# Kernel tuning notes

Measured on AMD Instinct MI355X. Metric: run time of the kernel, lower is better.

Reference implementation:

```python
import jax, jax.numpy as jnp
import numpy as np

WINDOWLEN = 8      # init arg windowlen
LOSS_THR = 120.0   # init arg losss
Q_BITS = 16


def ste_round(x):
    # Round with straight-through estimator (matches torch Round.apply)
    return x + jax.lax.stop_gradient(jnp.round(x) - x)


def delta_comp(x):
    # left-neighbor delta along width, zero-padded first column
    x_left = jnp.pad(x[:, :, :, :-1], ((0, 0), (0, 0), (0, 0), (1, 0)))
    return x - x_left, x_left


def part_quant(x, mx, mn, bw):
    neq = mx != mn
    denom = jnp.where(neq, mx - mn, jnp.ones((), x.dtype))
    scale = jnp.where(neq, (2.0 ** bw - 1.0) / denom, jnp.ones((), x.dtype))
    q = jnp.where(neq, ste_round((x - mn) * scale), x)
    return q, 1.0 / scale, jnp.where(neq, mn, jnp.zeros((), x.dtype))


def part_quant1(x, mx, bw):
    # en == 1 branch of the original
    lsb = 2.0 ** (ste_round(jnp.log2(mx / 2.0 ** (bw - 1))) + 1.0)
    return ste_round(x / lsb) * lsb


def setup_inputs() -> dict:
    key = jax.random.key(0)
    x = jax.random.normal(key, (1, 32, 1024, 1024), dtype=jnp.float32)
    return {"x": x}


def reference(x):
    w = WINDOWLEN
    batch, imgnum, height, width = x.shape
    # NOTE: the original also computes an 8-bit quantized delta (x_256) and
    # 2/4/8-bit masks, but these only feed print-statistics, never the output,
    # so they are omitted here.
    xd, x_left = delta_comp(x)
    In_max = xd.max()
    In_min = xd.min()
    q, s, m = part_quant(xd, In_max, In_min, Q_BITS)
    x1 = q * s + m  # dequantized delta
    Wb, Hb = width // w, height // w
    # --- block decomposition (replicates the torch reshape/permute chain) ---
    b = x1.reshape(batch, imgnum, height, Wb, w).transpose(0, 1, 3, 2, 4)
    c = b.reshape(batch, imgnum, Wb, Hb, w, w).transpose(0, 2, 3, 1, 4, 5)
    d = c.reshape(batch, Wb, Hb, imgnum, w * w).transpose(0, 1, 2, 4, 3)[0]  # [Wb,Hb,w*w,I]
    d1 = d.transpose(0, 1, 3, 2)  # [Wb,Hb,I,w*w]
    # --- 3x3 least-squares: fit each frame block from frames 0,1 + const ---
    a1 = d1[:, :, 0:1, :]
    a2 = d1[:, :, 1:2, :]
    a_base = jnp.concatenate([a1, a2, jnp.ones_like(a1)], axis=2)  # [Wb,Hb,3,w*w]
    degen = ((a1.max(3)[:, :, 0] - a1.min(3)[:, :, 0] < 1e-6)
             & (a2.max(3)[:, :, 0] - a2.min(3)[:, :, 0] < 1e-6))  # [Wb,Hb]
    a_t = a_base.transpose(0, 1, 3, 2)
    AT_A = a_base @ a_t  # [Wb,Hb,3,3]
    eye3 = jnp.eye(3, dtype=x.dtype)
    AT_A = jnp.where((jnp.linalg.det(AT_A) == 0)[..., None, None], eye3, AT_A)
    AT_A_inv = jnp.linalg.inv(AT_A)
    base = AT_A_inv @ a_base          # [Wb,Hb,3,w*w]
    p = base @ d                      # [Wb,Hb,3,I]
    r = a_t @ p                       # [Wb,Hb,w*w,I]
    r1 = part_quant1(r.transpose(0, 1, 3, 2), In_max, Q_BITS)  # [Wb,Hb,I,w*w]
    # --- per-(block,frame) accept/reject by MSE threshold ---
    loss_sum = ((d1 - r1) ** 2).sum(-1)  # [Wb,Hb,I]
    loss_sum = jnp.where(degen[..., None], LOSS_THR + 1.0, loss_sum)
    sel = loss_sum <= LOSS_THR
    rr = jnp.where(sel[..., None], r1, d1)
    rr = jnp.where(degen[..., None, None], d1, rr)  # rr[mask] = d1[mask]
    # --- reassemble image (reverse reshape chain) ---
    rr = rr.reshape(Wb, Hb, imgnum, w, w).transpose(2, 1, 3, 0, 4)
    rr = rr.reshape(imgnum, height, width)[None]
    return rr + x_left  # delta_dcom
```

## Files before the change

### kernel.cpp

```cpp
#include <hip/hip_runtime.h>
#include <math.h>

#define IMGN 32
#define HT 1024
#define WD 1024
#define IMG_STRIDE (HT*WD)
#define LOSS_THR_F 120.0f
#define MMX_BLOCKS 4096

#define IST 68
#define SST (32*IST + 8)

__global__ __launch_bounds__(256) void k_minmax(const float* __restrict__ x,
                                                float* __restrict__ wsf){
  const int lane = threadIdx.x & 63;
  const int wave_id = (blockIdx.x*256 + threadIdx.x) >> 6;
  const float4* x4 = (const float4*)x;
  const int base4 = wave_id * 512;

  float4 v[8];
  #pragma unroll
  for (int j = 0; j < 8; ++j) v[j] = x4[base4 + j*64 + lane];

  float lmin = INFINITY, lmax = -INFINITY;
  #pragma unroll
  for (int j = 0; j < 8; ++j){
    float lf = __shfl_up(v[j].w, 1);
    float carry = (j == 0 || j == 4) ? 0.0f : __shfl(v[j-1].w, 63);
    if (lane == 0) lf = carry;
    float d0 = v[j].x - lf,      d1 = v[j].y - v[j].x;
    float d2 = v[j].z - v[j].y,  d3 = v[j].w - v[j].z;
    lmin = fminf(lmin, fminf(fminf(d0, d1), fminf(d2, d3)));
    lmax = fmaxf(lmax, fmaxf(fmaxf(d0, d1), fmaxf(d2, d3)));
  }
  #pragma unroll
  for (int off = 32; off; off >>= 1){
    lmin = fminf(lmin, __shfl_xor(lmin, off));
    lmax = fmaxf(lmax, __shfl_xor(lmax, off));
  }
  __shared__ float smin[4], smax[4];
  int wv = threadIdx.x >> 6;
  if (lane == 0){ smin[wv] = lmin; smax[wv] = lmax; }
  __syncthreads();
  if (threadIdx.x == 0){
    wsf[2*blockIdx.x]   = fminf(fminf(smin[0], smin[1]), fminf(smin[2], smin[3]));
    wsf[2*blockIdx.x+1] = fmaxf(fmaxf(smax[0], smax[1]), fmaxf(smax[2], smax[3]));
  }
}

__global__ __launch_bounds__(256) void k_reduce(float* __restrict__ wsf){
  int t = threadIdx.x;
  float mn = INFINITY, mx = -INFINITY;
  #pragma unroll
  for (int j = 0; j < MMX_BLOCKS/256; ++j){
    float2 p = ((const float2*)wsf)[t + 256*j];
    mn = fminf(mn, p.x); mx = fmaxf(mx, p.y);
  }
  #pragma unroll
  for (int off = 32; off; off >>= 1){
    mn = fminf(mn, __shfl_xor(mn, off));
    mx = fmaxf(mx, __shfl_xor(mx, off));
  }
  __shared__ float smin[4], smax[4];
  int wv = t >> 6;
  if ((t & 63) == 0){ smin[wv] = mn; smax[wv] = mx; }
  __syncthreads();
  if (t == 0){
    wsf[2*MMX_BLOCKS]   = fminf(fminf(smin[0], smin[1]), fminf(smin[2], smin[3]));
    wsf[2*MMX_BLOCKS+1] = fmaxf(fmaxf(smax[0], smax[1]), fmaxf(smax[2], smax[3]));
  }
}

__global__ __launch_bounds__(512) void k_main(const float* __restrict__ x,
                                              float* __restrict__ out,
                                              const float* __restrict__ wsf){
  __shared__ __align__(16) float dsh[4*SST];
  __shared__ float s_inv[4][9];
  __shared__ int   s_degen[4];

  const int tid = threadIdx.x;
  const int bid = blockIdx.x;
  const int xcd = bid & 7;
  const int jj  = bid >> 3;
  const int hb  = xcd*16 + (jj >> 5);
  const int cb  = jj & 31;
  const int row0 = hb << 3;
  const int col0 = cb << 5;

  const float mn = wsf[2*MMX_BLOCKS];
  const float mx = wsf[2*MMX_BLOCKS+1];
  const bool  neq = (mx != mn);
  const float scale = neq ? (65535.0f / (mx - mn)) : 1.0f;
  const float sinv  = 1.0f / scale;
  const float moff  = neq ? mn : 0.0f;
  const float e1   = rintf(log2f(mx * (1.0f/32768.0f))) + 1.0f;
  const float lsb  = exp2f(e1);
  const float ilsb = exp2f(-e1);

  const int rem = tid & 63;
  const int r   = rem >> 3;
  const int fi  = rem & 7;
  const int i0  = tid >> 6;
  const int sB0 = fi >> 1;
  const int p1  = (r << 3) + ((fi & 1) << 2);
  const int lbase0 = sB0*SST + i0*IST + p1;
  const int gc0 = col0 + (fi << 2);
  const size_t elt0 = (size_t)i0*IMG_STRIDE + (size_t)(row0+r)*WD + gc0;

  float4 keep[4];
  #pragma unroll
  for (int k = 0; k < 4; ++k){
    const size_t elt = elt0 + (size_t)(k << 3)*IMG_STRIDE;
    float4 v = *(const float4*)(x + elt);
    float lf = __shfl_up(v.w, 1);
    if (fi == 0) lf = col0 ? x[elt - 1] : 0.0f;
    keep[k] = make_float4(lf, v.x, v.y, v.z);
    float d0 = v.x - lf, d1 = v.y - v.x, d2 = v.z - v.y, d3 = v.w - v.z;
    float q0, q1, q2, q3;
    if (neq){
      q0 = __fadd_rn(__fmul_rn(rintf((d0 - mn) * scale), sinv), moff);
      q1 = __fadd_rn(__fmul_rn(rintf((d1 - mn) * scale), sinv), moff);
      q2 = __fadd_rn(__fmul_rn(rintf((d2 - mn) * scale), sinv), moff);
      q3 = __fadd_rn(__fmul_rn(rintf((d3 - mn) * scale), sinv), moff);
    } else { q0 = d0; q1 = d1; q2 = d2; q3 = d3; }
    *(float4*)(dsh + lbase0 + k*(8*IST)) = make_float4(q0, q1, q2, q3);
  }
  __syncthreads();

  if (tid < 256){
    int s = tid >> 6;
    int p = tid & 63;
    float a0 = dsh[s*SST + 0*IST + p];
    float a1 = dsh[s*SST + 1*IST + p];
    double s00 = (double)a0*a0, s01 = (double)a0*a1, s02 = a0;
    double s11 = (double)a1*a1, s12 = a1;
    float mx0 = a0, mn0 = a0, mx1 = a1, mn1 = a1;
    #pragma unroll
    for (int off = 32; off; off >>= 1){
      s00 += __shfl_xor(s00, off);
      s01 += __shfl_xor(s01, off);
      s02 += __shfl_xor(s02, off);
      s11 += __shfl_xor(s11, off);
      s12 += __shfl_xor(s12, off);
      mx0 = fmaxf(mx0, __shfl_xor(mx0, off));
      mn0 = fminf(mn0, __shfl_xor(mn0, off));
      mx1 = fmaxf(mx1, __shfl_xor(mx1, off));
      mn1 = fminf(mn1, __shfl_xor(mn1, off));
    }
    if (p == 0){
      double a = (float)s00, b = (float)s01, c = (float)s02;
      double d = (float)s11, e = (float)s12, f = 64.0;
      double c00 = d*f - e*e;
      double c01 = c*e - b*f;
      double c02 = b*e - c*d;
      double det = a*c00 + b*c01 + c*c02;
      float inv[9];
      if (det == 0.0){
        inv[0]=1.f;inv[1]=0.f;inv[2]=0.f;
        inv[3]=0.f;inv[4]=1.f;inv[5]=0.f;
        inv[6]=0.f;inv[7]=0.f;inv[8]=1.f;
      } else {
        double id = 1.0/det;
        double c11 = a*f - c*c;
        double c12 = b*c - a*e;
        double c22 = a*d - b*b;
        inv[0]=(float)(c00*id); inv[1]=(float)(c01*id); inv[2]=(float)(c02*id);
        inv[3]=inv[1];          inv[4]=(float)(c11*id); inv[5]=(float)(c12*id);
        inv[6]=inv[2];          inv[7]=inv[5];          inv[8]=(float)(c22*id);
      }
      #pragma unroll
      for (int q = 0; q < 9; ++q) s_inv[s][q] = inv[q];
      s_degen[s] = (((mx0 - mn0) < 1e-6f) && ((mx1 - mn1) < 1e-6f)) ? 1 : 0;
    }
  }
  __syncthreads();

  const int i_img = (tid >> 3) & 31;
  const int sub   = tid & 7;
  const int p0    = sub << 3;

  float dv[2][8];
  int ss[2];
  #pragma unroll
  for (int k = 0; k < 2; ++k){
    const int sB = ((tid >> 8) << 1) + k; ss[k] = sB;
    const int sb = sB*SST;
    float4 dlo = *(const float4*)(dsh + sb + i_img*IST + p0);
    float4 dhi = *(const float4*)(dsh + sb + i_img*IST + p0 + 4);
    float4 A0l = *(const float4*)(dsh + sb + 0*IST + p0);
    float4 A0h = *(const float4*)(dsh + sb + 0*IST + p0 + 4);
    float4 A1l = *(const float4*)(dsh + sb + 1*IST + p0);
    float4 A1h = *(const float4*)(dsh + sb + 1*IST + p0 + 4);
    float dva[8] = {dlo.x,dlo.y,dlo.z,dlo.w, dhi.x,dhi.y,dhi.z,dhi.w};
    float a0a[8] = {A0l.x,A0l.y,A0l.z,A0l.w, A0h.x,A0h.y,A0h.z,A0h.w};
    float a1a[8] = {A1l.x,A1l.y,A1l.z,A1l.w, A1h.x,A1h.y,A1h.z,A1h.w};

    const float i00 = s_inv[sB][0], i01 = s_inv[sB][1], i02 = s_inv[sB][2];
    const float i10 = s_inv[sB][3], i11 = s_inv[sB][4], i12 = s_inv[sB][5];
    const float i20 = s_inv[sB][6], i21 = s_inv[sB][7], i22 = s_inv[sB][8];

    float pc0 = 0.f, pc1 = 0.f, pc2v = 0.f;
    #pragma unroll
    for (int c2 = 0; c2 < 8; ++c2){
      float b0 = __fadd_rn(__fmaf_rn(i01, a1a[c2], __fmul_rn(i00, a0a[c2])), i02);
      float b1 = __fadd_rn(__fmaf_rn(i11, a1a[c2], __fmul_rn(i10, a0a[c2])), i12);
      float b2 = __fadd_rn(__fmaf_rn(i21, a1a[c2], __fmul_rn(i20, a0a[c2])), i22);
      pc0  = __fmaf_rn(b0, dva[c2], pc0);
      pc1  = __fmaf_rn(b1, dva[c2], pc1);
      pc2v = __fmaf_rn(b2, dva[c2], pc2v);
    }
    pc0  += __shfl_xor(pc0, 1);  pc0  += __shfl_xor(pc0, 2);  pc0  += __shfl_xor(pc0, 4);
    pc1  += __shfl_xor(pc1, 1);  pc1  += __shfl_xor(pc1, 2);  pc1  += __shfl_xor(pc1, 4);
    pc2v += __shfl_xor(pc2v, 1); pc2v += __shfl_xor(pc2v, 2); pc2v += __shfl_xor(pc2v, 4);

    float r1v[8];
    float loss = 0.f;
    #pragma unroll
    for (int c2 = 0; c2 < 8; ++c2){
      float rv = __fadd_rn(__fmaf_rn(a1a[c2], pc1, __fmul_rn(a0a[c2], pc0)), pc2v);
      float r1 = __fmul_rn(rintf(__fmul_rn(rv, ilsb)), lsb);
      r1v[c2] = r1;
      float df = __fsub_rn(dva[c2], r1);
      loss = __fadd_rn(loss, __fmul_rn(df, df));
    }
    loss += __shfl_xor(loss, 1); loss += __shfl_xor(loss, 2); loss += __shfl_xor(loss, 4);
    const bool sel = (!s_degen[sB]) && (loss <= LOSS_THR_F);
    #pragma unroll
    for (int c2 = 0; c2 < 8; ++c2)
      dv[k][c2] = sel ? r1v[c2] : dva[c2];
  }
  __syncthreads();
  #pragma unroll
  for (int k = 0; k < 2; ++k){
    const int sb = ss[k]*SST + i_img*IST + p0;
    *(float4*)(dsh + sb)     = make_float4(dv[k][0], dv[k][1], dv[k][2], dv[k][3]);
    *(float4*)(dsh + sb + 4) = make_float4(dv[k][4], dv[k][5], dv[k][6], dv[k][7]);
  }
  __syncthreads();

  #pragma unroll
  for (int k = 0; k < 4; ++k){
    const size_t elt = elt0 + (size_t)(k << 3)*IMG_STRIDE;
    float4 q = *(const float4*)(dsh + lbase0 + k*(8*IST));
    float4 o;
    o.x = q.x + keep[k].x;
    o.y = q.y + keep[k].y;
    o.z = q.z + keep[k].z;
    o.w = q.w + keep[k].w;
    *(float4*)(out + elt) = o;
  }
}

extern "C" void kernel_launch(void* const* d_in, const int* in_sizes, int n_in,
                              void* d_out, int out_size, void* d_ws, size_t ws_size,
                              hipStream_t stream) {
  const float* x = (const float*)d_in[0];
  float* out = (float*)d_out;
  float* wsf = (float*)d_ws;
  hipLaunchKernelGGL(k_minmax, dim3(MMX_BLOCKS), dim3(256), 0, stream, x, wsf);
  hipLaunchKernelGGL(k_reduce, dim3(1),          dim3(256), 0, stream, wsf);
  hipLaunchKernelGGL(k_main,   dim3(4096),       dim3(512), 0, stream, x, out, wsf);
}
```

Before: 279.0 us.

## Fold global min/max reduction into main kernel and use nontemporal output stores

```diff
diff --git a/kernel.cpp b/kernel.cpp
--- a/kernel.cpp
+++ b/kernel.cpp
@@ -10,6 +10,8 @@
 
 #define IST 68
 #define SST (32*IST + 8)
+
+typedef float f4nt __attribute__((ext_vector_type(4)));
 
 __global__ __launch_bounds__(256) void k_minmax(const float* __restrict__ x,
                                                 float* __restrict__ wsf){
@@ -48,35 +50,13 @@
   }
 }
 
-__global__ __launch_bounds__(256) void k_reduce(float* __restrict__ wsf){
-  int t = threadIdx.x;
-  float mn = INFINITY, mx = -INFINITY;
-  #pragma unroll
-  for (int j = 0; j < MMX_BLOCKS/256; ++j){
-    float2 p = ((const float2*)wsf)[t + 256*j];
-    mn = fminf(mn, p.x); mx = fmaxf(mx, p.y);
-  }
-  #pragma unroll
-  for (int off = 32; off; off >>= 1){
-    mn = fminf(mn, __shfl_xor(mn, off));
-    mx = fmaxf(mx, __shfl_xor(mx, off));
-  }
-  __shared__ float smin[4], smax[4];
-  int wv = t >> 6;
-  if ((t & 63) == 0){ smin[wv] = mn; smax[wv] = mx; }
-  __syncthreads();
-  if (t == 0){
-    wsf[2*MMX_BLOCKS]   = fminf(fminf(smin[0], smin[1]), fminf(smin[2], smin[3]));
-    wsf[2*MMX_BLOCKS+1] = fmaxf(fmaxf(smax[0], smax[1]), fmaxf(smax[2], smax[3]));
-  }
-}
-
 __global__ __launch_bounds__(512) void k_main(const float* __restrict__ x,
                                               float* __restrict__ out,
                                               const float* __restrict__ wsf){
   __shared__ __align__(16) float dsh[4*SST];
   __shared__ float s_inv[4][9];
   __shared__ int   s_degen[4];
+  __shared__ float smm[16];
 
   const int tid = threadIdx.x;
   const int bid = blockIdx.x;
@@ -86,16 +66,6 @@
   const int cb  = jj & 31;
   const int row0 = hb << 3;
   const int col0 = cb << 5;
-
-  const float mn = wsf[2*MMX_BLOCKS];
-  const float mx = wsf[2*MMX_BLOCKS+1];
-  const bool  neq = (mx != mn);
-  const float scale = neq ? (65535.0f / (mx - mn)) : 1.0f;
-  const float sinv  = 1.0f / scale;
-  const float moff  = neq ? mn : 0.0f;
-  const float e1   = rintf(log2f(mx * (1.0f/32768.0f))) + 1.0f;
-  const float lsb  = exp2f(e1);
-  const float ilsb = exp2f(-e1);
 
   const int rem = tid & 63;
   const int r   = rem >> 3;
@@ -107,13 +77,52 @@
   const int gc0 = col0 + (fi << 2);
   const size_t elt0 = (size_t)i0*IMG_STRIDE + (size_t)(row0+r)*WD + gc0;
 
+  float4 vv[4];
+  #pragma unroll
+  for (int k = 0; k < 4; ++k)
+    vv[k] = *(const float4*)(x + elt0 + (size_t)(k << 3)*IMG_STRIDE);
+  float lfe[4] = {0.0f, 0.0f, 0.0f, 0.0f};
+  if (fi == 0 && col0){
+    #pragma unroll
+    for (int k = 0; k < 4; ++k)
+      lfe[k] = x[elt0 + (size_t)(k << 3)*IMG_STRIDE - 1];
+  }
+
+  float mnP = INFINITY, mxP = -INFINITY;
+  {
+    const float2* w2 = (const float2*)wsf;
+    #pragma unroll
+    for (int j = 0; j < 8; ++j){
+      float2 p = w2[tid + (j << 9)];
+      mnP = fminf(mnP, p.x); mxP = fmaxf(mxP, p.y);
+    }
+    #pragma unroll
+    for (int off = 32; off; off >>= 1){
+      mnP = fminf(mnP, __shfl_xor(mnP, off));
+      mxP = fmaxf(mxP, __shfl_xor(mxP, off));
+    }
+    if ((tid & 63) == 0){ smm[tid >> 6] = mnP; smm[8 + (tid >> 6)] = mxP; }
+  }
+  __syncthreads();
+  const float mn = fminf(fminf(fminf(smm[0], smm[1]), fminf(smm[2], smm[3])),
+                         fminf(fminf(smm[4], smm[5]), fminf(smm[6], smm[7])));
+  const float mx = fmaxf(fmaxf(fmaxf(smm[8], smm[9]), fmaxf(smm[10], smm[11])),
+                         fmaxf(fmaxf(smm[12], smm[13]), fmaxf(smm[14], smm[15])));
+
+  const bool  neq = (mx != mn);
+  const float scale = neq ? (65535.0f / (mx - mn)) : 1.0f;
+  const float sinv  = 1.0f / scale;
+  const float moff  = neq ? mn : 0.0f;
+  const float e1   = rintf(log2f(mx * (1.0f/32768.0f))) + 1.0f;
+  const float lsb  = exp2f(e1);
+  const float ilsb = exp2f(-e1);
+
   float4 keep[4];
   #pragma unroll
   for (int k = 0; k < 4; ++k){
-    const size_t elt = elt0 + (size_t)(k << 3)*IMG_STRIDE;
-    float4 v = *(const float4*)(x + elt);
+    float4 v = vv[k];
     float lf = __shfl_up(v.w, 1);
-    if (fi == 0) lf = col0 ? x[elt - 1] : 0.0f;
+    if (fi == 0) lf = lfe[k];
     keep[k] = make_float4(lf, v.x, v.y, v.z);
     float d0 = v.x - lf, d1 = v.y - v.x, d2 = v.z - v.y, d3 = v.w - v.z;
     float q0, q1, q2, q3;
@@ -242,12 +251,12 @@
   for (int k = 0; k < 4; ++k){
     const size_t elt = elt0 + (size_t)(k << 3)*IMG_STRIDE;
     float4 q = *(const float4*)(dsh + lbase0 + k*(8*IST));
-    float4 o;
+    f4nt o;
     o.x = q.x + keep[k].x;
     o.y = q.y + keep[k].y;
     o.z = q.z + keep[k].z;
     o.w = q.w + keep[k].w;
-    *(float4*)(out + elt) = o;
+    __builtin_nontemporal_store(o, (f4nt*)(out + elt));
   }
 }
 
@@ -258,6 +267,5 @@
   float* out = (float*)d_out;
   float* wsf = (float*)d_ws;
   hipLaunchKernelGGL(k_minmax, dim3(MMX_BLOCKS), dim3(256), 0, stream, x, wsf);
-  hipLaunchKernelGGL(k_reduce, dim3(1),          dim3(256), 0, stream, wsf);
   hipLaunchKernelGGL(k_main,   dim3(4096),       dim3(512), 0, stream, x, out, wsf);
 }
```

Measured after the change: 273.1 us. -2.1%, faster.
